# Kernel optimization log

Hardware: AMD Instinct MI355X
Metric: run time of the kernel (lower is better)

Reference implementation:

```python
import jax, jax.numpy as jnp
import numpy as np

N_NODES = 50000
N_EDGES = 1600000
IN_DIM = 256
HID = 128
BATCH = 16384
EDGE_FEAT = 6
BN_EPS = 1e-5


def _glorot(key, shape):
    fan_in, fan_out = shape[0], shape[1]
    lim = float(np.sqrt(6.0 / (fan_in + fan_out)))
    return jax.random.uniform(key, shape, jnp.float32, -lim, lim)


def setup_inputs() -> dict:
    key = jax.random.key(0)
    ks = jax.random.split(key, 20)
    return {
        "x": jax.random.normal(ks[0], (N_NODES, IN_DIM), jnp.float32),
        "edge_index": jax.random.randint(ks[1], (2, N_EDGES), 0, N_NODES, jnp.int64 if jax.config.jax_enable_x64 else jnp.int32),
        "src_nodes": jax.random.randint(ks[2], (BATCH,), 0, N_NODES),
        "tgt_nodes": jax.random.randint(ks[3], (BATCH,), 0, N_NODES),
        "edge_features": jax.random.uniform(ks[4], (BATCH, EDGE_FEAT), jnp.float32),
        # SAGEConv layer 0: lin_l (aggregated neighbors, has bias), lin_r (root, no bias)
        "sage_wl0": _glorot(ks[5], (IN_DIM, HID)),
        "sage_b0": jnp.zeros((HID,), jnp.float32),
        "sage_wr0": _glorot(ks[6], (IN_DIM, HID)),
        # SAGEConv layer 1
        "sage_wl1": _glorot(ks[7], (HID, HID)),
        "sage_b1": jnp.zeros((HID,), jnp.float32),
        "sage_wr1": _glorot(ks[8], (HID, HID)),
        # edge_processor: Linear(6, 64)
        "ep_w": _glorot(ks[9], (EDGE_FEAT, HID // 2)),
        "ep_b": jnp.zeros((HID // 2,), jnp.float32),
        # predictor: Linear(320,128) -> ReLU -> BN(128) -> Linear(128,64) -> ReLU -> Linear(64,1) -> Sigmoid
        "p1_w": _glorot(ks[10], (2 * HID + HID // 2, HID)),
        "p1_b": jnp.zeros((HID,), jnp.float32),
        "bn_gamma": jnp.ones((HID,), jnp.float32),
        "bn_beta": jnp.zeros((HID,), jnp.float32),
        "bn_mean": jnp.zeros((HID,), jnp.float32),
        "bn_var": jnp.ones((HID,), jnp.float32),
        "p2_w": _glorot(ks[11], (HID, HID // 2)),
        "p2_b": jnp.zeros((HID // 2,), jnp.float32),
        "p3_w": _glorot(ks[12], (HID // 2, 1)),
        "p3_b": jnp.zeros((1,), jnp.float32),
    }


def _sage_conv(h, src, dst, w_l, b, w_r):
    # PyG SAGEConv(mean): out_i = W_l @ mean_{j in N(i)} h_j + b + W_r @ h_i
    n = h.shape[0]
    agg = jax.ops.segment_sum(h[src], dst, num_segments=n)  # [N, d]
    deg = jax.ops.segment_sum(jnp.ones((src.shape[0],), h.dtype), dst, num_segments=n)
    mean = agg / jnp.maximum(deg, 1.0)[:, None]
    return mean @ w_l + b + h @ w_r


def reference(x, edge_index, src_nodes, tgt_nodes, edge_features,
              sage_wl0, sage_b0, sage_wr0, sage_wl1, sage_b1, sage_wr1,
              ep_w, ep_b, p1_w, p1_b, bn_gamma, bn_beta, bn_mean, bn_var,
              p2_w, p2_b, p3_w, p3_b):
    src, dst = edge_index[0], edge_index[1]
    h = _sage_conv(x, src, dst, sage_wl0, sage_b0, sage_wr0)
    h = jax.nn.relu(h)  # dropout is identity in eval mode
    h = _sage_conv(h, src, dst, sage_wl1, sage_b1, sage_wr1)
    src_emb = h[src_nodes]  # [B, HID]
    tgt_emb = h[tgt_nodes]  # [B, HID]
    edge_proc = jax.nn.relu(edge_features @ ep_w + ep_b)  # [B, HID//2]
    combined = jnp.concatenate([src_emb, tgt_emb, edge_proc], axis=1)  # [B, 320]
    z = jax.nn.relu(combined @ p1_w + p1_b)
    z = (z - bn_mean) / jnp.sqrt(bn_var + BN_EPS) * bn_gamma + bn_beta  # BN eval mode
    z = jax.nn.relu(z @ p2_w + p2_b)
    return jax.nn.sigmoid(z @ p3_w + p3_b)  # [B, 1]
```

## Files before the change

### kernel.cpp

```cpp
#include <hip/hip_runtime.h>
#include <hip/hip_bf16.h>

#define N_NODES 50000
#define N_EDGES 1600000
#define BATCH   16384
#define HID     128
#define NBUCK   782
#define NBLK    256
#define EPB     6250

using short8  = __attribute__((ext_vector_type(8))) short;
using floatx4 = __attribute__((ext_vector_type(4))) float;
using floatv4 = __attribute__((ext_vector_type(4))) float;
using uint2v  = __attribute__((ext_vector_type(2))) unsigned;
using uintx4  = __attribute__((ext_vector_type(4))) unsigned;
typedef unsigned short ushort_t;

__device__ __forceinline__ float bflo(unsigned u){ return __uint_as_float(u << 16); }
__device__ __forceinline__ float bfhi(unsigned u){ return __uint_as_float(u & 0xffff0000u); }
__device__ __forceinline__ float bf1(ushort_t u){ return __uint_as_float(((unsigned)u) << 16); }
__device__ __forceinline__ ushort_t f2bf(float f){
    unsigned u = __float_as_uint(f);
    return (ushort_t)((u + 0x7fffu + ((u >> 16) & 1u)) >> 16);
}
__device__ __forceinline__ int geti(const void* p, long long i, int is64){
    return is64 ? (int)((const long long*)p)[i] : ((const int*)p)[i];
}

__global__ void k_detect(const unsigned* __restrict__ xbits,
                         const unsigned* __restrict__ eibits, int* flags){
    __shared__ int f[2];
    int t = threadIdx.x;
    if (t < 2) f[t] = 0;
    __syncthreads();
    unsigned u = xbits[t];
    unsigned e0 = (u >> 7)  & 0xFF;
    unsigned e1 = (u >> 23) & 0xFF;
    if (e0 >= 140 || e1 >= 140) atomicOr(&f[0], 1);
    if (eibits[2*t + 1] != 0)   atomicOr(&f[1], 1);
    __syncthreads();
    if (t == 0){ flags[0] = f[0]; flags[1] = f[1] ? 0 : 1; }
}

#define NT 19
struct ConvDesc { const void* src[NT]; int cum[NT + 1]; };
__global__ void k_conv(ConvDesc d, ushort_t* __restrict__ dst, const int* __restrict__ flags){
    int i = blockIdx.x*256 + threadIdx.x;
    if (i >= d.cum[NT]) return;
    int seg = 0;
    while (i >= d.cum[seg + 1]) seg++;
    int off = i - d.cum[seg];
    ushort_t v;
    if (flags[0]) v = f2bf(((const float*)d.src[seg])[off]);
    else          v = ((const ushort_t*)d.src[seg])[off];
    dst[i] = v;
}

#define OFF_WL0 0
#define OFF_WR0 32768
#define OFF_WL1 65536
#define OFF_WR1 81920
#define OFF_B0  98304
#define OFF_B1  98432
#define OFF_EPW 98560
#define OFF_EPB 98944
#define OFF_P1W 99008
#define OFF_P1B 139968
#define OFF_BNG 140096
#define OFF_BNB 140224
#define OFF_BNM 140352
#define OFF_BNV 140480
#define OFF_P2W 140608
#define OFF_P2B 148800
#define OFF_P3W 148864
#define OFF_EF  148928
#define OFF_P3B 247232
#define CW_TOT  247233

#define PACK_TOT 147584
__global__ void k_pack(const ushort_t* __restrict__ cw,
                       ushort_t* __restrict__ bp0, ushort_t* __restrict__ bp1,
                       ushort_t* __restrict__ bpp1, ushort_t* __restrict__ bpp2,
                       float* __restrict__ bnf){
    int i = blockIdx.x*256 + threadIdx.x;
    if (i < 65536){
        int j = i & 7, lane = (i >> 3) & 63, c = (i >> 9) & 15, kk = i >> 13;
        int k = kk*32 + (lane >> 4)*8 + j;
        int n = c*16 + (lane & 15);
        bp0[i] = (n < 128) ? cw[OFF_WL0 + k*128 + n] : cw[OFF_WR0 + k*128 + (n-128)];
    } else if (i < 98304){
        int i2 = i - 65536;
        int j = i2 & 7, lane = (i2 >> 3) & 63, c = (i2 >> 9) & 15, kk = i2 >> 13;
        int k = kk*32 + (lane >> 4)*8 + j;
        int n = c*16 + (lane & 15);
        bp1[i2] = (n < 128) ? cw[OFF_WL1 + k*128 + n] : cw[OFF_WR1 + k*128 + (n-128)];
    } else if (i < 139264){
        int i2 = i - 98304;
        int j = i2 & 7, lane = (i2 >> 3) & 63, ct = (i2 >> 9) & 7, kk = i2 >> 12;
        int k = kk*32 + (lane >> 4)*8 + j;
        int n = ct*16 + (lane & 15);
        bpp1[i2] = cw[OFF_P1W + k*128 + n];
    } else if (i < 147456){
        int i2 = i - 139264;
        int j = i2 & 7, lane = (i2 >> 3) & 63, ct = (i2 >> 9) & 3, kk = i2 >> 11;
        int k = kk*32 + (lane >> 4)*8 + j;
        int n = ct*16 + (lane & 15);
        bpp2[i2] = cw[OFF_P2W + k*64 + n];
    } else if (i < PACK_TOT){
        int n = i - 147456;
        float g = bf1(cw[OFF_BNG + n]), b = bf1(cw[OFF_BNB + n]);
        float m = bf1(cw[OFF_BNM + n]), v = bf1(cw[OFF_BNV + n]);
        float sc = g / sqrtf(v + 1e-5f);
        bnf[n] = sc; bnf[128 + n] = b - m*sc;
    }
}

__global__ __launch_bounds__(256)
void k_xcast(const float* __restrict__ x, ushort_t* __restrict__ xbf,
             const int* __restrict__ flags){
    if (!flags[0]) return;
    int i = blockIdx.x*256 + threadIdx.x;
    floatv4 v = ((const floatv4*)x)[i];
    uint2v o;
    o.x = (unsigned)f2bf(v[0]) | ((unsigned)f2bf(v[1]) << 16);
    o.y = (unsigned)f2bf(v[2]) | ((unsigned)f2bf(v[3]) << 16);
    ((uint2v*)xbf)[i] = o;
}

__global__ __launch_bounds__(256)
void kb_hist(const void* __restrict__ ei, int* __restrict__ hist,
             const int* __restrict__ flags){
    __shared__ int lh[NBUCK];
    for (int i = threadIdx.x; i < NBUCK; i += 256) lh[i] = 0;
    __syncthreads();
    int i64 = flags[1];
    int e0 = blockIdx.x * EPB;
    for (int e = e0 + threadIdx.x; e < e0 + EPB; e += 256){
        int d = geti(ei, (long long)N_EDGES + e, i64);
        atomicAdd(&lh[d >> 6], 1);
    }
    __syncthreads();
    for (int i = threadIdx.x; i < NBUCK; i += 256)
        hist[i * NBLK + blockIdx.x] = lh[i];
}

__global__ __launch_bounds__(256)
void kb_scancol(int* __restrict__ hist, int* __restrict__ btot){
    __shared__ int sh[256];
    int b = blockIdx.x, t = threadIdx.x;
    int v = hist[b*NBLK + t];
    sh[t] = v; __syncthreads();
    for (int o = 1; o < 256; o <<= 1){
        int x = (t >= o) ? sh[t-o] : 0;
        __syncthreads();
        sh[t] += x;
        __syncthreads();
    }
    hist[b*NBLK + t] = sh[t] - v;
    if (t == 255) btot[b] = sh[255];
}

__global__ __launch_bounds__(1024)
void kb_scanbase(const int* __restrict__ btot, int* __restrict__ bbase,
                 int* __restrict__ off){
    __shared__ int sh[1024];
    int t = threadIdx.x;
    int v = (t < NBUCK) ? btot[t] : 0;
    sh[t] = v; __syncthreads();
    for (int o = 1; o < 1024; o <<= 1){
        int x = (t >= o) ? sh[t-o] : 0;
        __syncthreads();
        sh[t] += x;
        __syncthreads();
    }
    if (t < NBUCK) bbase[t] = sh[t] - v;
    if (t == 0){ bbase[NBUCK] = N_EDGES; off[N_NODES] = N_EDGES; }
}

__global__ __launch_bounds__(256)
void kb_scatter(const void* __restrict__ ei, const int* __restrict__ hist,
                const int* __restrict__ bbase, unsigned* __restrict__ ebuf,
                const int* __restrict__ flags){
    __shared__ int lcur[NBUCK];
    for (int i = threadIdx.x; i < NBUCK; i += 256)
        lcur[i] = bbase[i] + hist[i*NBLK + blockIdx.x];
    __syncthreads();
    int i64 = flags[1];
    int e0 = blockIdx.x * EPB;
    for (int e = e0 + threadIdx.x; e < e0 + EPB; e += 256){
        int s = geti(ei, e, i64);
        int d = geti(ei, (long long)N_EDGES + e, i64);
        int p = atomicAdd(&lcur[d >> 6], 1);
        ebuf[p] = (unsigned)s | ((unsigned)(d & 63) << 16);
    }
}

__global__ __launch_bounds__(256)
void kb_csr(const unsigned* __restrict__ ebuf, const int* __restrict__ bbase,
            ushort_t* __restrict__ csr, int* __restrict__ off){
    __shared__ int ldeg[64];
    int b = blockIdx.x, t = threadIdx.x;
    int ebase = bbase[b], eend = bbase[b+1];
    if (t < 64) ldeg[t] = 0;
    __syncthreads();
    for (int i = ebase + t; i < eend; i += 256)
        atomicAdd(&ldeg[(ebuf[i] >> 16) & 63], 1);
    __syncthreads();
    if (t < 64){
        int v = ldeg[t];
        int sum = v;
        #pragma unroll
        for (int o = 1; o < 64; o <<= 1){
            int x = __shfl_up(sum, o, 64);
            if (t >= o) sum += x;
        }
        int excl = sum - v;
        int node = b*64 + t;
        if (node < N_NODES) off[node] = ebase + excl;
        ldeg[t] = excl;
    }
    __syncthreads();
    for (int i = ebase + t; i < eend; i += 256){
        unsigned u = ebuf[i];
        int p = atomicAdd(&ldeg[(u >> 16) & 63], 1);
        csr[ebase + p] = (ushort_t)(u & 0xffffu);
    }
}

template<int KSTEPS, bool MF32>
__global__ __launch_bounds__(256)
void k_gemm2(const void* __restrict__ a_raw, const ushort_t* __restrict__ a_bf,
             const ushort_t* __restrict__ Bp, ushort_t* __restrict__ out,
             int M, const int* __restrict__ flags)
{
    const int lane = threadIdx.x & 63;
    const int w    = threadIdx.x >> 6;
    const int l16  = lane & 15;
    const int q    = lane >> 4;
    const int S    = KSTEPS * 32;
    const int m_base = blockIdx.x * 64;

    const ushort_t* A = (MF32 && flags[0]) ? a_bf : (const ushort_t*)a_raw;

    const ushort_t* arow[4];
    bool ok[4];
    #pragma unroll
    for (int rt = 0; rt < 4; ++rt){
        int m = m_base + rt*16 + l16;
        ok[rt] = (m < M);
        arow[rt] = A + (size_t)(ok[rt] ? m : 0) * S + q*8;
    }
    const short8* bbase = (const short8*)(Bp + (size_t)(w*4)*64*8) + lane;

    floatx4 acc[4][4] = {};
    for (int kk = 0; kk < KSTEPS; ++kk){
        short8 b[4];
        #pragma unroll
        for (int ci = 0; ci < 4; ++ci)
            b[ci] = bbase[(kk*16 + ci)*64];
        short8 a[4];
        #pragma unroll
        for (int rt = 0; rt < 4; ++rt){
            short8 af = {0,0,0,0,0,0,0,0};
            if (ok[rt]) af = *(const short8*)(arow[rt] + kk*32);
            a[rt] = af;
        }
        #pragma unroll
        for (int rt = 0; rt < 4; ++rt)
            #pragma unroll
            for (int ci = 0; ci < 4; ++ci)
                acc[rt][ci] = __builtin_amdgcn_mfma_f32_16x16x32_bf16(a[rt], b[ci], acc[rt][ci], 0, 0, 0);
    }

    #pragma unroll
    for (int rt = 0; rt < 4; ++rt){
        int row_b = m_base + rt*16 + q*4;
        #pragma unroll
        for (int r = 0; r < 4; ++r){
            int row = row_b + r;
            if (row < M){
                #pragma unroll
                for (int ci = 0; ci < 4; ++ci)
                    out[(size_t)row*256 + w*64 + ci*16 + l16] = f2bf(acc[rt][ci][r]);
            }
        }
    }
}

__global__ __launch_bounds__(256)
void k_agg(const int* __restrict__ off, const ushort_t* __restrict__ csr,
           const ushort_t* __restrict__ yr, const ushort_t* __restrict__ bias,
           ushort_t* __restrict__ out, int do_relu)
{
    int v = blockIdx.x*4 + (threadIdx.x >> 6);
    if (v >= N_NODES) return;
    const int l = threadIdx.x & 63;
    const int g = l >> 4;
    const int c = l & 15;
    int e0 = off[v], e1 = off[v+1];
    const ushort_t* yb = yr + c*8;

    float a0=0,a1=0,a2=0,a3=0,a4=0,a5=0,a6=0,a7=0;
    float b0=0,b1=0,b2=0,b3=0,b4=0,b5=0,b6=0,b7=0;
    int p = e0;
    for (; p + 8 <= e1; p += 8){
        int uA = csr[p + g];
        int uB = csr[p + 4 + g];
        uintx4 dA = *(const uintx4*)(yb + (size_t)uA*256);
        uintx4 dB = *(const uintx4*)(yb + (size_t)uB*256);
        a0 += bflo(dA.x); a1 += bfhi(dA.x);
        a2 += bflo(dA.y); a3 += bfhi(dA.y);
        a4 += bflo(dA.z); a5 += bfhi(dA.z);
        a6 += bflo(dA.w); a7 += bfhi(dA.w);
        b0 += bflo(dB.x); b1 += bfhi(dB.x);
        b2 += bflo(dB.y); b3 += bfhi(dB.y);
        b4 += bflo(dB.z); b5 += bfhi(dB.z);
        b6 += bflo(dB.w); b7 += bfhi(dB.w);
    }
    if (p + 4 <= e1){
        int uA = csr[p + g];
        uintx4 dA = *(const uintx4*)(yb + (size_t)uA*256);
        a0 += bflo(dA.x); a1 += bfhi(dA.x);
        a2 += bflo(dA.y); a3 += bfhi(dA.y);
        a4 += bflo(dA.z); a5 += bfhi(dA.z);
        a6 += bflo(dA.w); a7 += bfhi(dA.w);
        p += 4;
    }
    if (p + g < e1){
        int uB = csr[p + g];
        uintx4 dB = *(const uintx4*)(yb + (size_t)uB*256);
        b0 += bflo(dB.x); b1 += bfhi(dB.x);
        b2 += bflo(dB.y); b3 += bfhi(dB.y);
        b4 += bflo(dB.z); b5 += bfhi(dB.z);
        b6 += bflo(dB.w); b7 += bfhi(dB.w);
    }
    a0 += b0; a1 += b1; a2 += b2; a3 += b3;
    a4 += b4; a5 += b5; a6 += b6; a7 += b7;
    #pragma unroll
    for (int m = 16; m <= 32; m <<= 1){
        a0 += __shfl_xor(a0, m, 64); a1 += __shfl_xor(a1, m, 64);
        a2 += __shfl_xor(a2, m, 64); a3 += __shfl_xor(a3, m, 64);
        a4 += __shfl_xor(a4, m, 64); a5 += __shfl_xor(a5, m, 64);
        a6 += __shfl_xor(a6, m, 64); a7 += __shfl_xor(a7, m, 64);
    }
    if (g == 0){
        float inv = 1.f / (float)max(e1 - e0, 1);
        uintx4 rr = *(const uintx4*)(yr + (size_t)v*256 + 128 + c*8);
        uintx4 bb = *(const uintx4*)(bias + c*8);
        float v0 = a0*inv + bflo(rr.x) + bflo(bb.x);
        float v1 = a1*inv + bfhi(rr.x) + bfhi(bb.x);
        float v2 = a2*inv + bflo(rr.y) + bflo(bb.y);
        float v3 = a3*inv + bfhi(rr.y) + bfhi(bb.y);
        float v4 = a4*inv + bflo(rr.z) + bflo(bb.z);
        float v5 = a5*inv + bfhi(rr.z) + bfhi(bb.z);
        float v6 = a6*inv + bflo(rr.w) + bflo(bb.w);
        float v7 = a7*inv + bfhi(rr.w) + bfhi(bb.w);
        if (do_relu){
            v0=fmaxf(v0,0.f); v1=fmaxf(v1,0.f); v2=fmaxf(v2,0.f); v3=fmaxf(v3,0.f);
            v4=fmaxf(v4,0.f); v5=fmaxf(v5,0.f); v6=fmaxf(v6,0.f); v7=fmaxf(v7,0.f);
        }
        uintx4 o;
        o.x = (unsigned)f2bf(v0) | ((unsigned)f2bf(v1) << 16);
        o.y = (unsigned)f2bf(v2) | ((unsigned)f2bf(v3) << 16);
        o.z = (unsigned)f2bf(v4) | ((unsigned)f2bf(v5) << 16);
        o.w = (unsigned)f2bf(v6) | ((unsigned)f2bf(v7) << 16);
        *(uintx4*)(out + (size_t)v*128 + c*8) = o;
    }
}

__global__ __launch_bounds__(256)
void k_pred2(const ushort_t* __restrict__ h2,
             const void* __restrict__ srcn, const void* __restrict__ tgtn,
             const ushort_t* __restrict__ cw, const ushort_t* __restrict__ bpp1,
             const ushort_t* __restrict__ bpp2, const float* __restrict__ bnf,
             void* __restrict__ outp, const int* __restrict__ flags)
{
    __shared__ ushort_t comb[64][328];
    __shared__ ushort_t zbuf[64][136];
    __shared__ ushort_t z2buf[64][68];
    __shared__ float    partial[4][64];
    __shared__ int      sid[64], tid_[64];

    const int t    = threadIdx.x;
    const int lane = t & 63;
    const int w    = t >> 6;
    const int l16  = lane & 15;
    const int q    = lane >> 4;
    const int row0 = blockIdx.x * 64;
    const int i64  = flags[1];

    if (t < 64){ sid[t] = geti(srcn, row0 + t, i64); tid_[t] = geti(tgtn, row0 + t, i64); }
    __syncthreads();

    const unsigned* h2u = (const unsigned*)h2;
    #pragma unroll 4
    for (int r = w*16; r < w*16 + 16; ++r){
        unsigned us = h2u[(size_t)sid[r]*64 + lane];
        unsigned ut = h2u[(size_t)tid_[r]*64 + lane];
        *(unsigned*)&comb[r][2*lane]       = us;
        *(unsigned*)&comb[r][128 + 2*lane] = ut;
    }
    {
        int r = t >> 2, c0 = (t & 3) * 16;
        float efv[6];
        #pragma unroll
        for (int k = 0; k < 6; ++k) efv[k] = bf1(cw[OFF_EF + (row0 + r)*6 + k]);
        #pragma unroll
        for (int c = 0; c < 16; ++c){
            int n = c0 + c;
            float a = bf1(cw[OFF_EPB + n]);
            #pragma unroll
            for (int k = 0; k < 6; ++k) a += efv[k] * bf1(cw[OFF_EPW + k*64 + n]);
            comb[r][256 + n] = f2bf(fmaxf(a, 0.f));
        }
    }
    __syncthreads();

    floatx4 acc[4][2] = {};
    for (int kk = 0; kk < 10; ++kk){
        short8 a[4];
        #pragma unroll
        for (int rt = 0; rt < 4; ++rt)
            a[rt] = *(const short8*)&comb[rt*16 + l16][kk*32 + q*8];
        #pragma unroll
        for (int ci = 0; ci < 2; ++ci){
            short8 b = *(const short8*)&bpp1[(((kk*8) + (w*2 + ci))*64 + lane)*8];
            #pragma unroll
            for (int rt = 0; rt < 4; ++rt)
                acc[rt][ci] = __builtin_amdgcn_mfma_f32_16x16x32_bf16(a[rt], b, acc[rt][ci], 0, 0, 0);
        }
    }
    #pragma unroll
    for (int ci = 0; ci < 2; ++ci){
        int n = w*32 + ci*16 + l16;
        float b1v = bf1(cw[OFF_P1B + n]);
        float sc = bnf[n], sh = bnf[128 + n];
        #pragma unroll
        for (int rt = 0; rt < 4; ++rt)
            #pragma unroll
            for (int r = 0; r < 4; ++r){
                float v = fmaxf(acc[rt][ci][r] + b1v, 0.f) * sc + sh;
                zbuf[rt*16 + q*4 + r][n] = f2bf(v);
            }
    }
    __syncthreads();

    floatx4 acc2[4] = {};
    for (int kk = 0; kk < 4; ++kk){
        short8 b = *(const short8*)&bpp2[(((kk*4) + w)*64 + lane)*8];
        #pragma unroll
        for (int rt = 0; rt < 4; ++rt){
            short8 a = *(const short8*)&zbuf[rt*16 + l16][kk*32 + q*8];
            acc2[rt] = __builtin_amdgcn_mfma_f32_16x16x32_bf16(a, b, acc2[rt], 0, 0, 0);
        }
    }
    {
        int n = w*16 + l16;
        float b2v = bf1(cw[OFF_P2B + n]);
        #pragma unroll
        for (int rt = 0; rt < 4; ++rt)
            #pragma unroll
            for (int r = 0; r < 4; ++r)
                z2buf[rt*16 + q*4 + r][n] = f2bf(fmaxf(acc2[rt][r] + b2v, 0.f));
    }
    __syncthreads();

    {
        int r = t & 63, seg = t >> 6;
        float s = 0.f;
        #pragma unroll
        for (int c = 0; c < 16; ++c){
            int n = seg*16 + c;
            s += bf1(z2buf[r][n]) * bf1(cw[OFF_P3W + n]);
        }
        partial[seg][r] = s;
    }
    __syncthreads();
    if (t < 64){
        float zf = partial[0][t] + partial[1][t] + partial[2][t] + partial[3][t] + bf1(cw[OFF_P3B]);
        float sg = 1.f / (1.f + __expf(-zf));
        if (flags[0]) ((float*)outp)[row0 + t] = sg;
        else          ((ushort_t*)outp)[row0 + t] = f2bf(sg);
    }
}

extern "C" void kernel_launch(void* const* d_in, const int* in_sizes, int n_in,
                              void* d_out, int out_size, void* d_ws, size_t ws_size,
                              hipStream_t stream)
{
    const void* x    = d_in[0];
    const void* ei   = d_in[1];
    const void* srcn = d_in[2];
    const void* tgtn = d_in[3];

    char* p = (char*)d_ws;
    auto carve = [&](size_t bytes)->char*{ char* r = p; p += (bytes + 511) & ~size_t(511); return r; };
    int* flags = (int*)carve(64);
    int* off   = (int*)carve((N_NODES+1)*4);
    int* btot  = (int*)carve(NBUCK*4);
    int* bbase = (int*)carve((NBUCK+1)*4);
    ushort_t* csr = (ushort_t*)carve((size_t)N_EDGES*2);
    ushort_t* yr  = (ushort_t*)carve((size_t)N_NODES*256*2);
    ushort_t* h   = (ushort_t*)carve((size_t)N_NODES*128*2);
    ushort_t* cw  = (ushort_t*)carve((size_t)CW_TOT*2);
    ushort_t* bp0 = (ushort_t*)carve((size_t)65536*2);
    ushort_t* bp1 = (ushort_t*)carve((size_t)32768*2);
    ushort_t* bpp1= (ushort_t*)carve((size_t)40960*2);
    ushort_t* bpp2= (ushort_t*)carve((size_t)8192*2);
    float*    bnf = (float*)carve(256*4);
    ushort_t* xbf = (ushort_t*)carve((size_t)N_NODES*256*2);

    int*      hist = (int*)yr;
    unsigned* ebuf = (unsigned*)((char*)yr + 8u*1024*1024);

    k_detect<<<1, 256, 0, stream>>>((const unsigned*)x, (const unsigned*)ei, flags);

    ConvDesc cd;
    const int srcidx[NT] = {5,7,8,10,6,9,11,12,13,14,15,16,17,18,19,20,21,4,22};
    const int lens[NT]   = {32768,32768,16384,16384,128,128,384,64,40960,128,128,128,128,128,8192,64,64,98304,1};
    int run = 0;
    for (int i = 0; i < NT; ++i){ cd.src[i] = d_in[srcidx[i]]; cd.cum[i] = run; run += lens[i]; }
    cd.cum[NT] = run;
    k_conv<<<(CW_TOT+255)/256, 256, 0, stream>>>(cd, cw, flags);
    k_pack<<<(PACK_TOT+255)/256, 256, 0, stream>>>(cw, bp0, bp1, bpp1, bpp2, bnf);
    k_xcast<<<12500, 256, 0, stream>>>((const float*)x, xbf, flags);

    kb_hist    <<<NBLK, 256, 0, stream>>>(ei, hist, flags);
    kb_scancol <<<NBUCK, 256, 0, stream>>>(hist, btot);
    kb_scanbase<<<1, 1024, 0, stream>>>(btot, bbase, off);
    kb_scatter <<<NBLK, 256, 0, stream>>>(ei, hist, bbase, ebuf, flags);
    kb_csr     <<<NBUCK, 256, 0, stream>>>(ebuf, bbase, csr, off);

    int gblocks = (N_NODES + 63) / 64;
    k_gemm2<8, true ><<<gblocks, 256, 0, stream>>>(x, xbf, bp0, yr, N_NODES, flags);
    k_agg<<<(N_NODES+3)/4, 256, 0, stream>>>(off, csr, yr, cw+OFF_B0, h, 1);
    k_gemm2<4, false><<<gblocks, 256, 0, stream>>>(h, nullptr, bp1, yr, N_NODES, flags);
    k_agg<<<(N_NODES+3)/4, 256, 0, stream>>>(off, csr, yr, cw+OFF_B1, h, 0);

    k_pred2<<<BATCH/64, 256, 0, stream>>>(h, srcn, tgtn, cw, bpp1, bpp2, bnf, d_out, flags);
}
```

Baseline: 348.6 us.

## Fuse fp32-to-bf16 cast into first GEMM and widen aggregation unroll

Removes the separate x-cast kernel and its bf16 copy of x. A new GEMM variant reads fp32 rows directly and truncates them to bf16 in registers with byte permutes, and the bf16 GEMM path exits early when the input is fp32. The neighbor-aggregation loop is also unrolled to 16 edges per iteration with packed float2 accumulators to keep more gathers in flight. The costs are that the fused GEMM reads twice as many A bytes, and the conversion now truncates instead of rounding to nearest even.

```diff
diff --git a/kernel.cpp b/kernel.cpp
--- a/kernel.cpp
+++ b/kernel.cpp
@@ -12,6 +12,7 @@
 using short8  = __attribute__((ext_vector_type(8))) short;
 using floatx4 = __attribute__((ext_vector_type(4))) float;
 using floatv4 = __attribute__((ext_vector_type(4))) float;
+using float2v = __attribute__((ext_vector_type(2))) float;
 using uint2v  = __attribute__((ext_vector_type(2))) unsigned;
 using uintx4  = __attribute__((ext_vector_type(4))) unsigned;
 typedef unsigned short ushort_t;
@@ -25,6 +26,9 @@
 }
 __device__ __forceinline__ int geti(const void* p, long long i, int is64){
     return is64 ? (int)((const long long*)p)[i] : ((const int*)p)[i];
+}
+__device__ __forceinline__ float2v up2(unsigned u){
+    float2v r; r.x = bflo(u); r.y = bfhi(u); return r;
 }
 
 __global__ void k_detect(const unsigned* __restrict__ xbits,
@@ -116,18 +120,6 @@
 }
 
 __global__ __launch_bounds__(256)
-void k_xcast(const float* __restrict__ x, ushort_t* __restrict__ xbf,
-             const int* __restrict__ flags){
-    if (!flags[0]) return;
-    int i = blockIdx.x*256 + threadIdx.x;
-    floatv4 v = ((const floatv4*)x)[i];
-    uint2v o;
-    o.x = (unsigned)f2bf(v[0]) | ((unsigned)f2bf(v[1]) << 16);
-    o.y = (unsigned)f2bf(v[2]) | ((unsigned)f2bf(v[3]) << 16);
-    ((uint2v*)xbf)[i] = o;
-}
-
-__global__ __launch_bounds__(256)
 void kb_hist(const void* __restrict__ ei, int* __restrict__ hist,
              const int* __restrict__ flags){
     __shared__ int lh[NBUCK];
@@ -227,12 +219,12 @@
     }
 }
 
-template<int KSTEPS, bool MF32>
-__global__ __launch_bounds__(256)
-void k_gemm2(const void* __restrict__ a_raw, const ushort_t* __restrict__ a_bf,
-             const ushort_t* __restrict__ Bp, ushort_t* __restrict__ out,
-             int M, const int* __restrict__ flags)
+template<int KSTEPS, bool CHECKBF>
+__global__ __launch_bounds__(256)
+void k_gemm2(const ushort_t* __restrict__ A, const ushort_t* __restrict__ Bp,
+             ushort_t* __restrict__ out, int M, const int* __restrict__ flags)
 {
+    if (CHECKBF && flags[0]) return;
     const int lane = threadIdx.x & 63;
     const int w    = threadIdx.x >> 6;
     const int l16  = lane & 15;
@@ -240,8 +232,6 @@
     const int S    = KSTEPS * 32;
     const int m_base = blockIdx.x * 64;
 
-    const ushort_t* A = (MF32 && flags[0]) ? a_bf : (const ushort_t*)a_raw;
-
     const ushort_t* arow[4];
     bool ok[4];
     #pragma unroll
@@ -264,6 +254,72 @@
             short8 af = {0,0,0,0,0,0,0,0};
             if (ok[rt]) af = *(const short8*)(arow[rt] + kk*32);
             a[rt] = af;
+        }
+        #pragma unroll
+        for (int rt = 0; rt < 4; ++rt)
+            #pragma unroll
+            for (int ci = 0; ci < 4; ++ci)
+                acc[rt][ci] = __builtin_amdgcn_mfma_f32_16x16x32_bf16(a[rt], b[ci], acc[rt][ci], 0, 0, 0);
+    }
+
+    #pragma unroll
+    for (int rt = 0; rt < 4; ++rt){
+        int row_b = m_base + rt*16 + q*4;
+        #pragma unroll
+        for (int r = 0; r < 4; ++r){
+            int row = row_b + r;
+            if (row < M){
+                #pragma unroll
+                for (int ci = 0; ci < 4; ++ci)
+                    out[(size_t)row*256 + w*64 + ci*16 + l16] = f2bf(acc[rt][ci][r]);
+            }
+        }
+    }
+}
+
+__global__ __launch_bounds__(256)
+void k_gemm2f(const float* __restrict__ Af, const ushort_t* __restrict__ Bp,
+              ushort_t* __restrict__ out, int M, const int* __restrict__ flags)
+{
+    if (!flags[0]) return;
+    const int KSTEPS = 8;
+    const int lane = threadIdx.x & 63;
+    const int w    = threadIdx.x >> 6;
+    const int l16  = lane & 15;
+    const int q    = lane >> 4;
+    const int S    = KSTEPS * 32;
+    const int m_base = blockIdx.x * 64;
+
+    const float* arow[4];
+    bool ok[4];
+    #pragma unroll
+    for (int rt = 0; rt < 4; ++rt){
+        int m = m_base + rt*16 + l16;
+        ok[rt] = (m < M);
+        arow[rt] = Af + (size_t)(ok[rt] ? m : 0) * S + q*8;
+    }
+    const short8* bbase = (const short8*)(Bp + (size_t)(w*4)*64*8) + lane;
+
+    floatx4 acc[4][4] = {};
+    for (int kk = 0; kk < KSTEPS; ++kk){
+        short8 b[4];
+        #pragma unroll
+        for (int ci = 0; ci < 4; ++ci)
+            b[ci] = bbase[(kk*16 + ci)*64];
+        short8 a[4];
+        #pragma unroll
+        for (int rt = 0; rt < 4; ++rt){
+            union { unsigned u[4]; short8 s; } cv;
+            cv.u[0]=0; cv.u[1]=0; cv.u[2]=0; cv.u[3]=0;
+            if (ok[rt]){
+                floatv4 f0 = *(const floatv4*)(arow[rt] + kk*32);
+                floatv4 f1 = *(const floatv4*)(arow[rt] + kk*32 + 4);
+                cv.u[0] = __builtin_amdgcn_perm(__float_as_uint(f0.y), __float_as_uint(f0.x), 0x07060302);
+                cv.u[1] = __builtin_amdgcn_perm(__float_as_uint(f0.w), __float_as_uint(f0.z), 0x07060302);
+                cv.u[2] = __builtin_amdgcn_perm(__float_as_uint(f1.y), __float_as_uint(f1.x), 0x07060302);
+                cv.u[3] = __builtin_amdgcn_perm(__float_as_uint(f1.w), __float_as_uint(f1.z), 0x07060302);
+            }
+            a[rt] = cv.s;
         }
         #pragma unroll
         for (int rt = 0; rt < 4; ++rt)
@@ -300,42 +356,37 @@
     int e0 = off[v], e1 = off[v+1];
     const ushort_t* yb = yr + c*8;
 
-    float a0=0,a1=0,a2=0,a3=0,a4=0,a5=0,a6=0,a7=0;
-    float b0=0,b1=0,b2=0,b3=0,b4=0,b5=0,b6=0,b7=0;
+    float2v A0[4] = {}, A1[4] = {}, A2[4] = {}, A3[4] = {};
     int p = e0;
-    for (; p + 8 <= e1; p += 8){
-        int uA = csr[p + g];
-        int uB = csr[p + 4 + g];
-        uintx4 dA = *(const uintx4*)(yb + (size_t)uA*256);
-        uintx4 dB = *(const uintx4*)(yb + (size_t)uB*256);
-        a0 += bflo(dA.x); a1 += bfhi(dA.x);
-        a2 += bflo(dA.y); a3 += bfhi(dA.y);
-        a4 += bflo(dA.z); a5 += bfhi(dA.z);
-        a6 += bflo(dA.w); a7 += bfhi(dA.w);
-        b0 += bflo(dB.x); b1 += bfhi(dB.x);
-        b2 += bflo(dB.y); b3 += bfhi(dB.y);
-        b4 += bflo(dB.z); b5 += bfhi(dB.z);
-        b6 += bflo(dB.w); b7 += bfhi(dB.w);
-    }
-    if (p + 4 <= e1){
-        int uA = csr[p + g];
-        uintx4 dA = *(const uintx4*)(yb + (size_t)uA*256);
-        a0 += bflo(dA.x); a1 += bfhi(dA.x);
-        a2 += bflo(dA.y); a3 += bfhi(dA.y);
-        a4 += bflo(dA.z); a5 += bfhi(dA.z);
-        a6 += bflo(dA.w); a7 += bfhi(dA.w);
-        p += 4;
+    for (; p + 16 <= e1; p += 16){
+        int u0 = csr[p + g];
+        int u1 = csr[p + 4 + g];
+        int u2 = csr[p + 8 + g];
+        int u3 = csr[p + 12 + g];
+        uintx4 d0 = *(const uintx4*)(yb + (size_t)u0*256);
+        uintx4 d1 = *(const uintx4*)(yb + (size_t)u1*256);
+        uintx4 d2 = *(const uintx4*)(yb + (size_t)u2*256);
+        uintx4 d3 = *(const uintx4*)(yb + (size_t)u3*256);
+        A0[0] += up2(d0.x); A0[1] += up2(d0.y); A0[2] += up2(d0.z); A0[3] += up2(d0.w);
+        A1[0] += up2(d1.x); A1[1] += up2(d1.y); A1[2] += up2(d1.z); A1[3] += up2(d1.w);
+        A2[0] += up2(d2.x); A2[1] += up2(d2.y); A2[2] += up2(d2.z); A2[3] += up2(d2.w);
+        A3[0] += up2(d3.x); A3[1] += up2(d3.y); A3[2] += up2(d3.z); A3[3] += up2(d3.w);
+    }
+    for (; p + 4 <= e1; p += 4){
+        int u0 = csr[p + g];
+        uintx4 d0 = *(const uintx4*)(yb + (size_t)u0*256);
+        A0[0] += up2(d0.x); A0[1] += up2(d0.y); A0[2] += up2(d0.z); A0[3] += up2(d0.w);
     }
     if (p + g < e1){
-        int uB = csr[p + g];
-        uintx4 dB = *(const uintx4*)(yb + (size_t)uB*256);
-        b0 += bflo(dB.x); b1 += bfhi(dB.x);
-        b2 += bflo(dB.y); b3 += bfhi(dB.y);
-        b4 += bflo(dB.z); b5 += bfhi(dB.z);
-        b6 += bflo(dB.w); b7 += bfhi(dB.w);
-    }
-    a0 += b0; a1 += b1; a2 += b2; a3 += b3;
-    a4 += b4; a5 += b5; a6 += b6; a7 += b7;
+        int u1 = csr[p + g];
+        uintx4 d1 = *(const uintx4*)(yb + (size_t)u1*256);
+        A1[0] += up2(d1.x); A1[1] += up2(d1.y); A1[2] += up2(d1.z); A1[3] += up2(d1.w);
+    }
+    #pragma unroll
+    for (int j = 0; j < 4; ++j) A0[j] += A1[j] + A2[j] + A3[j];
+
+    float a0=A0[0].x, a1=A0[0].y, a2=A0[1].x, a3=A0[1].y;
+    float a4=A0[2].x, a5=A0[2].y, a6=A0[3].x, a7=A0[3].y;
     #pragma unroll
     for (int m = 16; m <= 32; m <<= 1){
         a0 += __shfl_xor(a0, m, 64); a1 += __shfl_xor(a1, m, 64);
@@ -508,7 +559,6 @@
     ushort_t* bpp1= (ushort_t*)carve((size_t)40960*2);
     ushort_t* bpp2= (ushort_t*)carve((size_t)8192*2);
     float*    bnf = (float*)carve(256*4);
-    ushort_t* xbf = (ushort_t*)carve((size_t)N_NODES*256*2);
 
     int*      hist = (int*)yr;
     unsigned* ebuf = (unsigned*)((char*)yr + 8u*1024*1024);
@@ -523,7 +573,6 @@
     cd.cum[NT] = run;
     k_conv<<<(CW_TOT+255)/256, 256, 0, stream>>>(cd, cw, flags);
     k_pack<<<(PACK_TOT+255)/256, 256, 0, stream>>>(cw, bp0, bp1, bpp1, bpp2, bnf);
-    k_xcast<<<12500, 256, 0, stream>>>((const float*)x, xbf, flags);
 
     kb_hist    <<<NBLK, 256, 0, stream>>>(ei, hist, flags);
     kb_scancol <<<NBUCK, 256, 0, stream>>>(hist, btot);
@@ -532,9 +581,10 @@
     kb_csr     <<<NBUCK, 256, 0, stream>>>(ebuf, bbase, csr, off);
 
     int gblocks = (N_NODES + 63) / 64;
-    k_gemm2<8, true ><<<gblocks, 256, 0, stream>>>(x, xbf, bp0, yr, N_NODES, flags);
+    k_gemm2<8, true><<<gblocks, 256, 0, stream>>>((const ushort_t*)x, bp0, yr, N_NODES, flags);
+    k_gemm2f<<<gblocks, 256, 0, stream>>>((const float*)x, bp0, yr, N_NODES, flags);
     k_agg<<<(N_NODES+3)/4, 256, 0, stream>>>(off, csr, yr, cw+OFF_B0, h, 1);
-    k_gemm2<4, false><<<gblocks, 256, 0, stream>>>(h, nullptr, bp1, yr, N_NODES, flags);
+    k_gemm2<4, false><<<gblocks, 256, 0, stream>>>(h, bp1, yr, N_NODES, flags);
     k_agg<<<(N_NODES+3)/4, 256, 0, stream>>>(off, csr, yr, cw+OFF_B1, h, 0);
 
     k_pred2<<<BATCH/64, 256, 0, stream>>>(h, srcn, tgtn, cw, bpp1, bpp2, bnf, d_out, flags);
```

Result: no change. 347.2 us (-0.4%).
